# Kernel tuning notes

Hardware: AMD Instinct MI355X
Metric: run time of the kernel (lower is better)

## Reference

```python
import jax, jax.numpy as jnp
import numpy as np

B, T, IN, H, OUT = 128, 512, 64, 1024, 1


def _glorot(key, shape, fan_in):
    # mimic nn.Linear default init scale (uniform +-1/sqrt(fan_in))
    bound = 1.0 / np.sqrt(fan_in)
    return jax.random.uniform(key, shape, jnp.float32, -bound, bound)


def setup_inputs() -> dict:
    key = jax.random.key(0)
    ks = jax.random.split(key, 20)
    inp = {
        "x": jax.random.normal(ks[0], (B, T, IN), jnp.float32),
        "boundary": jax.random.normal(ks[1], (B, 2), jnp.float32),
        # layer 0: stacked gate weights, order [i, f, o, g]
        "Wx0": _glorot(ks[2], (4 * H, IN), IN),
        "bx0": _glorot(ks[3], (4 * H,), IN),
        "Uh0": _glorot(ks[4], (4 * H, H), H),
        "bh0": _glorot(ks[5], (4 * H,), H),
        "Wb0": _glorot(ks[6], (H, 2), 2),
        "bb0": _glorot(ks[7], (H,), 2),
        # layer 1
        "Wx1": _glorot(ks[8], (4 * H, H), H),
        "bx1": _glorot(ks[9], (4 * H,), H),
        "Uh1": _glorot(ks[10], (4 * H, H), H),
        "bh1": _glorot(ks[11], (4 * H,), H),
        "Wb1": _glorot(ks[12], (H, 2), 2),
        "bb1": _glorot(ks[13], (H, 2)[:1], 2),
        # output head
        "fcW": _glorot(ks[14], (OUT, H), H),
        "fcb": _glorot(ks[15], (OUT,), H),
    }
    return inp


def _cell(gates, f_extra, c_prev):
    # gates: [B, 4H] pre-activations in order i,f,o,g
    i, f, o, g = jnp.split(gates, 4, axis=-1)
    i = jax.nn.sigmoid(i)
    f = jax.nn.sigmoid(f + f_extra)
    o = jax.nn.sigmoid(o)
    g = jnp.tanh(g)
    c = f * c_prev + i * g
    h = o * jnp.tanh(c)
    return h, c


def reference(x, boundary, Wx0, bx0, Uh0, bh0, Wb0, bb0,
              Wx1, bx1, Uh1, bh1, Wb1, bb1, fcW, fcb):
    batch = x.shape[0]
    Hdim = fcW.shape[1]
    # precompute input projections for layer 0 over all timesteps: [T,B,4H]
    xp0 = jnp.einsum('bti,gi->tbg', x, Wx0) + bx0
    # boundary influence on forget gate, constant over time: [B,H]
    bi0 = boundary @ Wb0.T + bb0
    bi1 = boundary @ Wb1.T + bb1

    zeros = jnp.zeros((batch, Hdim), x.dtype)
    carry0 = (zeros, zeros, zeros, zeros)  # h0, c0, h1, c1

    def step(carry, xp_t):
        h0, c0, h1, c1 = carry
        g0 = xp_t + h0 @ Uh0.T + bh0
        h0n, c0n = _cell(g0, bi0, c0)
        g1 = h0n @ Wx1.T + bx1 + h1 @ Uh1.T + bh1
        h1n, c1n = _cell(g1, bi1, c1)
        return (h0n, c0n, h1n, c1n), None

    (h0, c0, h1, c1), _ = jax.lax.scan(step, carry0, xp0)
    # fc applied to last timestep's top-layer hidden state
    return h1 @ fcW.T + fcb
```

## Files before the change

### kernel.cpp

```cpp
#include <hip/hip_runtime.h>
#include <math.h>


#define Hd 1024
#define Bd 128
#define Td 512
#define INd 64
#define NWG 256
#define NTHR 512

typedef _Float16 f16;
typedef _Float16 half8 __attribute__((ext_vector_type(8)));
typedef float f32x4 __attribute__((ext_vector_type(4)));


__global__ __launch_bounds__(512) void init_state(
    const float* __restrict__ bnd, const float* __restrict__ Wb0,
    const float* __restrict__ bb0, const float* __restrict__ Wb1,
    const float* __restrict__ bb1,
    float* __restrict__ bi0, float* __restrict__ bi1,
    f16* __restrict__ h0buf, f16* __restrict__ h1buf,
    unsigned int* __restrict__ sync)
{
    int idx = blockIdx.x * 512 + threadIdx.x;
    int b = idx >> 10;
    int h = idx & 1023;
    float b0v = bnd[b * 2 + 0], b1v = bnd[b * 2 + 1];
    bi0[idx] = b0v * Wb0[h * 2 + 0] + b1v * Wb0[h * 2 + 1] + bb0[h];
    bi1[idx] = b0v * Wb1[h * 2 + 0] + b1v * Wb1[h * 2 + 1] + bb1[h];
    h0buf[idx] = (f16)0.f;  h0buf[idx + Bd * Hd] = (f16)0.f;
    h1buf[idx] = (f16)0.f;  h1buf[idx + Bd * Hd] = (f16)0.f;
    if (idx < 640) sync[idx] = 0u;
}

__global__ __launch_bounds__(512) void xpose(
    const float* __restrict__ x, f16* __restrict__ xT)
{
    int idx = blockIdx.x * 512 + threadIdx.x;
    int b = idx >> 15;
    int t = (idx >> 6) & 511;
    int i = idx & 63;
    xT[((size_t)t * Bd + b) * INd + i] = (f16)x[idx];
}

__global__ __launch_bounds__(NTHR, 2) void lstm_persist(
    const f16* __restrict__ xT,
    f16* __restrict__ h0buf, f16* __restrict__ h1buf,
    const float* __restrict__ bi0, const float* __restrict__ bi1,
    const float* __restrict__ Wx0, const float* __restrict__ bx0,
    const float* __restrict__ Uh0, const float* __restrict__ bh0,
    const float* __restrict__ Wx1, const float* __restrict__ bx1,
    const float* __restrict__ Uh1, const float* __restrict__ bh1,
    const float* __restrict__ fcW, const float* __restrict__ fcb,
    float* __restrict__ out, unsigned int* __restrict__ sync)
{
    const int tid  = threadIdx.x;
    const int w    = tid >> 6;
    const int lane = tid & 63;
    const int n    = lane & 15;
    const int q    = lane >> 4;
    const int wg   = blockIdx.x;
    const int c0wg = wg * 4;
    const int hcol = c0wg + (n & 3);
    const int gid  = n >> 2;
    const bool lowhalf = (w < 4);
    const int p    = lowhalf ? w : (w - 4);
    const int mt   = lowhalf ? 2 * p : 2 * p + 1;
    const size_t S = (size_t)Bd * Hd;

    __shared__ f16 B0[16 * 1096];
    __shared__ float xchg[3072];

    const bool glead = ((wg & 31) == 0);
    unsigned int* garr = sync + 32 + 32 * (wg >> 5);
    int  xcd  = 0;
    bool lead = false;
    unsigned int* relp = nullptr;
    if (tid == 0) {
        asm volatile("s_getreg_b32 %0, hwreg(HW_REG_XCC_ID)" : "=s"(xcd));
        xcd &= 7;
        unsigned r = __hip_atomic_fetch_add(&sync[608 + xcd], 1u,
                         __ATOMIC_RELAXED, __HIP_MEMORY_SCOPE_AGENT);
        lead = (r == 0u);
        relp = sync + 288 + 32 * xcd;
    }

    {
        int nr = tid >> 5;
        int gr = (nr >> 2) * Hd + c0wg + (nr & 3);
        for (int k = tid & 31; k < 1088; k += 32) {
            float v = (k < Hd) ? Uh0[(size_t)gr * Hd + k]
                               : Wx0[(size_t)gr * INd + (k - Hd)];
            B0[nr * 1096 + k] = (f16)v;
        }
    }

    half8 b1f[32];
    {
        const float* Wsrc = lowhalf ? Wx1 : Uh1;
        int gr = gid * Hd + c0wg + (n & 3);
        const float* rp = Wsrc + (size_t)gr * Hd + q * 8;
        #pragma unroll
        for (int kk = 0; kk < 32; ++kk) {
            half8 hv;
            #pragma unroll
            for (int j = 0; j < 8; ++j) hv[j] = (f16)rp[kk * 32 + j];
            b1f[kk] = hv;
        }
    }

    float gb0[4], gb1[4], bia0[4], bia1[4];
    #pragma unroll
    for (int g = 0; g < 4; ++g) {
        gb0[g] = bx0[g * Hd + hcol] + bh0[g * Hd + hcol];
        gb1[g] = bx1[g * Hd + hcol] + bh1[g * Hd + hcol];
    }
    #pragma unroll
    for (int r = 0; r < 4; ++r) {
        int row = mt * 16 + q * 4 + r;
        bia0[r] = bi0[row * Hd + hcol];
        bia1[r] = bi1[row * Hd + hcol];
    }
    f32x4 c0v = {0.f, 0.f, 0.f, 0.f};
    f32x4 c1v = {0.f, 0.f, 0.f, 0.f};

    __syncthreads();

    unsigned epoch = 0;

    for (int s = -1; s <= 511; ++s) {
        const bool do_l0 = (s < 511);
        const bool do_l1 = (s >= 0);
        const int pr = s & 1;
        const f16* h0r = h0buf + (size_t)pr * S;
        f16*       h0w = h0buf + (size_t)(1 - pr) * S;
        const f16* h1r = h1buf + (size_t)(1 - pr) * S;
        f16*       h1w = h1buf + (size_t)pr * S;

        f32x4 a0a = {0.f,0.f,0.f,0.f}, a0b = {0.f,0.f,0.f,0.f};
        f32x4 a1a = {0.f,0.f,0.f,0.f}, a1b = {0.f,0.f,0.f,0.f};

        if (lowhalf) {
            const half8* pA0 = (const half8*)(h0r + (size_t)(2*p*16 + n) * Hd + q*8);
            const half8* pA1 = (const half8*)(h0r + (size_t)((2*p+1)*16 + n) * Hd + q*8);
            const half8* pB  = (const half8*)(&B0[n * 1096 + q * 8]);
            if (do_l0 && do_l1) {
                #pragma unroll
                for (int kk = 0; kk < 32; ++kk) {
                    half8 A0 = pA0[kk*4], A1 = pA1[kk*4], Bl = pB[kk*4];
                    a0a = __builtin_amdgcn_mfma_f32_16x16x32_f16(A0, Bl, a0a, 0,0,0);
                    a0b = __builtin_amdgcn_mfma_f32_16x16x32_f16(A1, Bl, a0b, 0,0,0);
                    a1a = __builtin_amdgcn_mfma_f32_16x16x32_f16(A0, b1f[kk], a1a, 0,0,0);
                    a1b = __builtin_amdgcn_mfma_f32_16x16x32_f16(A1, b1f[kk], a1b, 0,0,0);
                }
            } else if (do_l0) {
                #pragma unroll
                for (int kk = 0; kk < 32; ++kk) {
                    half8 A0 = pA0[kk*4], A1 = pA1[kk*4], Bl = pB[kk*4];
                    a0a = __builtin_amdgcn_mfma_f32_16x16x32_f16(A0, Bl, a0a, 0,0,0);
                    a0b = __builtin_amdgcn_mfma_f32_16x16x32_f16(A1, Bl, a0b, 0,0,0);
                }
            } else {
                #pragma unroll
                for (int kk = 0; kk < 32; ++kk) {
                    half8 A0 = pA0[kk*4], A1 = pA1[kk*4];
                    a1a = __builtin_amdgcn_mfma_f32_16x16x32_f16(A0, b1f[kk], a1a, 0,0,0);
                    a1b = __builtin_amdgcn_mfma_f32_16x16x32_f16(A1, b1f[kk], a1b, 0,0,0);
                }
            }
            if (do_l0) {
                const f16* xt = xT + (size_t)(s + 1) * Bd * INd;
                const half8* pX0 = (const half8*)(xt + (size_t)(2*p*16 + n) * INd + q*8);
                const half8* pX1 = (const half8*)(xt + (size_t)((2*p+1)*16 + n) * INd + q*8);
                #pragma unroll
                for (int kk = 0; kk < 2; ++kk) {
                    half8 Bl = pB[(32 + kk) * 4];
                    a0a = __builtin_amdgcn_mfma_f32_16x16x32_f16(pX0[kk*4], Bl, a0a, 0,0,0);
                    a0b = __builtin_amdgcn_mfma_f32_16x16x32_f16(pX1[kk*4], Bl, a0b, 0,0,0);
                }
            }
        } else if (do_l1) {
            const half8* pH1a = (const half8*)(h1r + (size_t)(2*p*16 + n) * Hd + q*8);
            const half8* pH1b = (const half8*)(h1r + (size_t)((2*p+1)*16 + n) * Hd + q*8);
            #pragma unroll
            for (int kk = 0; kk < 32; ++kk) {
                half8 A0 = pH1a[kk*4], A1 = pH1b[kk*4];
                a1a = __builtin_amdgcn_mfma_f32_16x16x32_f16(A0, b1f[kk], a1a, 0,0,0);
                a1b = __builtin_amdgcn_mfma_f32_16x16x32_f16(A1, b1f[kk], a1b, 0,0,0);
            }
        }

        float* slotA = xchg;
        float* slotB = xchg + 1024;
        float* slotC = xchg + 2048;
        if (lowhalf) {
            if (do_l0) *(f32x4*)&slotA[p * 256 + lane * 4] = a0b;
            if (do_l1) *(f32x4*)&slotB[p * 256 + lane * 4] = a1b;
        } else {
            if (do_l1) *(f32x4*)&slotC[p * 256 + lane * 4] = a1a;
        }
        __syncthreads();

        f32x4 g0acc, g1acc;
        if (lowhalf) {
            g0acc = a0a;
            if (do_l1) g1acc = a1a + *(const f32x4*)&slotC[p * 256 + lane * 4];
        } else {
            if (do_l0) g0acc = *(const f32x4*)&slotA[p * 256 + lane * 4];
            if (do_l1) g1acc = a1b + *(const f32x4*)&slotB[p * 256 + lane * 4];
        }

        auto cell = [&](f32x4 acc, const float* gb, const float* bia,
                        f32x4& cst, f16* hw) {
            #pragma unroll
            for (int r = 0; r < 4; ++r) {
                float own = acc[r];
                float v4  = __shfl_xor(own, 4);
                float v8  = __shfl_xor(own, 8);
                float v12 = __shfl_xor(own, 12);
                float ip = gid==0?own: gid==1?v4 : gid==2?v8 : v12;
                float fp = gid==0?v4 : gid==1?own: gid==2?v12: v8;
                float op = gid==0?v8 : gid==1?v12: gid==2?own: v4;
                float gp = gid==0?v12: gid==1?v8 : gid==2?v4 : own;
                float I = 1.f / (1.f + expf(-(ip + gb[0])));
                float F = 1.f / (1.f + expf(-(fp + gb[1] + bia[r])));
                float O = 1.f / (1.f + expf(-(op + gb[2])));
                float G = tanhf(gp + gb[3]);
                float c = F * cst[r] + I * G;
                cst[r] = c;
                float h = O * tanhf(c);
                if (n < 4) {
                    union { f16 hf; unsigned short us; } cv; cv.hf = (f16)h;
                    __hip_atomic_store(
                        (unsigned short*)&hw[(size_t)(mt * 16 + q * 4 + r) * Hd + c0wg + n],
                        cv.us, __ATOMIC_RELAXED, __HIP_MEMORY_SCOPE_AGENT);
                }
            }
        };
        if (do_l0) cell(g0acc, gb0, bia0, c0v, h0w);
        if (do_l1) cell(g1acc, gb1, bia1, c1v, h1w);

        __syncthreads();
        if (tid == 0) {
            const unsigned tgt = epoch + 1u;
            __hip_atomic_fetch_add(garr, 1u, __ATOMIC_RELAXED,
                                   __HIP_MEMORY_SCOPE_AGENT);
            if (glead) {
                while (__hip_atomic_load(garr, __ATOMIC_RELAXED,
                                         __HIP_MEMORY_SCOPE_AGENT) < 32u * tgt)
                    __builtin_amdgcn_s_sleep(1);
                __hip_atomic_fetch_add(sync, 32u, __ATOMIC_RELAXED,
                                       __HIP_MEMORY_SCOPE_AGENT);
            }
            if (lead) {
                while (__hip_atomic_load(sync, __ATOMIC_RELAXED,
                                         __HIP_MEMORY_SCOPE_AGENT) < NWG * tgt)
                    __builtin_amdgcn_s_sleep(1);
                asm volatile("buffer_inv sc1\n\ts_waitcnt vmcnt(0)" ::: "memory");
                __hip_atomic_store(relp, tgt, __ATOMIC_RELAXED,
                                   __HIP_MEMORY_SCOPE_AGENT);
            } else {
                while (__hip_atomic_load(relp, __ATOMIC_RELAXED,
                                         __HIP_MEMORY_SCOPE_AGENT) < tgt)
                    __builtin_amdgcn_s_sleep(1);
                asm volatile("buffer_inv\n\ts_waitcnt vmcnt(0)" ::: "memory");
            }
        }
        epoch++;
        __syncthreads();
    }

    if (blockIdx.x < Bd) {
        int b = blockIdx.x;
        const f16* hf = h1buf + S + (size_t)b * Hd;
        int k = tid * 2;
        float sum = (float)hf[k] * fcW[k] + (float)hf[k + 1] * fcW[k + 1];
        #pragma unroll
        for (int off = 32; off > 0; off >>= 1) sum += __shfl_down(sum, off);
        float* red = xchg;
        if (lane == 0) red[w] = sum;
        __syncthreads();
        if (tid == 0) {
            float t = 0.f;
            #pragma unroll
            for (int i = 0; i < 8; ++i) t += red[i];
            out[b] = t + fcb[0];
        }
    }
}

extern "C" void kernel_launch(void* const* d_in, const int* in_sizes, int n_in,
                              void* d_out, int out_size, void* d_ws, size_t ws_size,
                              hipStream_t stream) {
    const float* x        = (const float*)d_in[0];
    const float* boundary = (const float*)d_in[1];
    const float* Wx0      = (const float*)d_in[2];
    const float* bx0      = (const float*)d_in[3];
    const float* Uh0      = (const float*)d_in[4];
    const float* bh0      = (const float*)d_in[5];
    const float* Wb0      = (const float*)d_in[6];
    const float* bb0      = (const float*)d_in[7];
    const float* Wx1      = (const float*)d_in[8];
    const float* bx1      = (const float*)d_in[9];
    const float* Uh1      = (const float*)d_in[10];
    const float* bh1      = (const float*)d_in[11];
    const float* Wb1      = (const float*)d_in[12];
    const float* bb1      = (const float*)d_in[13];
    const float* fcW      = (const float*)d_in[14];
    const float* fcb      = (const float*)d_in[15];
    float* out = (float*)d_out;

    char* ws = (char*)d_ws;
    f16*   xT    = (f16*)(ws);
    f16*   h0buf = (f16*)(ws + 8388608);
    f16*   h1buf = (f16*)(ws + 8912896);
    float* bi0   = (float*)(ws + 9437184);
    float* bi1   = (float*)(ws + 9961472);
    unsigned int* sync = (unsigned int*)(ws + 10485760);

    init_state<<<256, 512, 0, stream>>>(boundary, Wb0, bb0, Wb1, bb1,
                                        bi0, bi1, h0buf, h1buf, sync);
    xpose<<<8192, 512, 0, stream>>>(x, xT);

    void* args[] = {
        (void*)&xT, (void*)&h0buf, (void*)&h1buf, (void*)&bi0, (void*)&bi1,
        (void*)&Wx0, (void*)&bx0, (void*)&Uh0, (void*)&bh0,
        (void*)&Wx1, (void*)&bx1, (void*)&Uh1, (void*)&bh1,
        (void*)&fcW, (void*)&fcb, (void*)&out, (void*)&sync
    };
    hipLaunchCooperativeKernel((void*)lstm_persist, dim3(NWG), dim3(NTHR),
                               args, 0, stream);
}
```

Baseline: 11.62 ms.

## Store hidden state in k-blocked layout and use fast sigmoid/tanh intrinsics

Changes the global h0/h1 exchange buffers from row-major [B][H] to a blocked [H/4][B][4] layout. Each workgroup's 4-column output slice now lands in one contiguous region, and the MFMA A-operand is built from two half4 loads. The gate nonlinearities switch from expf/tanhf to __expf/__fdividef approximations, which shortens the serial per-step cell math at some accuracy cost. The final FC readout is updated to index the new layout.

```diff
diff --git a/kernel.cpp b/kernel.cpp
--- a/kernel.cpp
+++ b/kernel.cpp
@@ -11,8 +11,16 @@
 
 typedef _Float16 f16;
 typedef _Float16 half8 __attribute__((ext_vector_type(8)));
+typedef _Float16 half4 __attribute__((ext_vector_type(4)));
 typedef float f32x4 __attribute__((ext_vector_type(4)));
 
+
+__device__ __forceinline__ float fsigm(float x) {
+    return __fdividef(1.f, 1.f + __expf(-x));
+}
+__device__ __forceinline__ float ftanh_(float x) {
+    return 1.f - __fdividef(2.f, 1.f + __expf(2.f * x));
+}
 
 __global__ __launch_bounds__(512) void init_state(
     const float* __restrict__ bnd, const float* __restrict__ Wb0,
@@ -128,6 +136,9 @@
 
     unsigned epoch = 0;
 
+    const int ra = 2 * p * 16 + n;
+    const int rb = (2 * p + 1) * 16 + n;
+
     for (int s = -1; s <= 511; ++s) {
         const bool do_l0 = (s < 511);
         const bool do_l1 = (s >= 0);
@@ -141,13 +152,19 @@
         f32x4 a1a = {0.f,0.f,0.f,0.f}, a1b = {0.f,0.f,0.f,0.f};
 
         if (lowhalf) {
-            const half8* pA0 = (const half8*)(h0r + (size_t)(2*p*16 + n) * Hd + q*8);
-            const half8* pA1 = (const half8*)(h0r + (size_t)((2*p+1)*16 + n) * Hd + q*8);
+            const half4* hb = (const half4*)h0r;
             const half8* pB  = (const half8*)(&B0[n * 1096 + q * 8]);
             if (do_l0 && do_l1) {
                 #pragma unroll
                 for (int kk = 0; kk < 32; ++kk) {
-                    half8 A0 = pA0[kk*4], A1 = pA1[kk*4], Bl = pB[kk*4];
+                    int kb = q * 2 + kk * 8;
+                    half4 a0lo = hb[(kb    ) * 128 + ra];
+                    half4 a0hi = hb[(kb + 1) * 128 + ra];
+                    half4 a1lo = hb[(kb    ) * 128 + rb];
+                    half4 a1hi = hb[(kb + 1) * 128 + rb];
+                    half8 A0 = __builtin_shufflevector(a0lo, a0hi, 0,1,2,3,4,5,6,7);
+                    half8 A1 = __builtin_shufflevector(a1lo, a1hi, 0,1,2,3,4,5,6,7);
+                    half8 Bl = pB[kk*4];
                     a0a = __builtin_amdgcn_mfma_f32_16x16x32_f16(A0, Bl, a0a, 0,0,0);
                     a0b = __builtin_amdgcn_mfma_f32_16x16x32_f16(A1, Bl, a0b, 0,0,0);
                     a1a = __builtin_amdgcn_mfma_f32_16x16x32_f16(A0, b1f[kk], a1a, 0,0,0);
@@ -156,14 +173,27 @@
             } else if (do_l0) {
                 #pragma unroll
                 for (int kk = 0; kk < 32; ++kk) {
-                    half8 A0 = pA0[kk*4], A1 = pA1[kk*4], Bl = pB[kk*4];
+                    int kb = q * 2 + kk * 8;
+                    half4 a0lo = hb[(kb    ) * 128 + ra];
+                    half4 a0hi = hb[(kb + 1) * 128 + ra];
+                    half4 a1lo = hb[(kb    ) * 128 + rb];
+                    half4 a1hi = hb[(kb + 1) * 128 + rb];
+                    half8 A0 = __builtin_shufflevector(a0lo, a0hi, 0,1,2,3,4,5,6,7);
+                    half8 A1 = __builtin_shufflevector(a1lo, a1hi, 0,1,2,3,4,5,6,7);
+                    half8 Bl = pB[kk*4];
                     a0a = __builtin_amdgcn_mfma_f32_16x16x32_f16(A0, Bl, a0a, 0,0,0);
                     a0b = __builtin_amdgcn_mfma_f32_16x16x32_f16(A1, Bl, a0b, 0,0,0);
                 }
             } else {
                 #pragma unroll
                 for (int kk = 0; kk < 32; ++kk) {
-                    half8 A0 = pA0[kk*4], A1 = pA1[kk*4];
+                    int kb = q * 2 + kk * 8;
+                    half4 a0lo = hb[(kb    ) * 128 + ra];
+                    half4 a0hi = hb[(kb + 1) * 128 + ra];
+                    half4 a1lo = hb[(kb    ) * 128 + rb];
+                    half4 a1hi = hb[(kb + 1) * 128 + rb];
+                    half8 A0 = __builtin_shufflevector(a0lo, a0hi, 0,1,2,3,4,5,6,7);
+                    half8 A1 = __builtin_shufflevector(a1lo, a1hi, 0,1,2,3,4,5,6,7);
                     a1a = __builtin_amdgcn_mfma_f32_16x16x32_f16(A0, b1f[kk], a1a, 0,0,0);
                     a1b = __builtin_amdgcn_mfma_f32_16x16x32_f16(A1, b1f[kk], a1b, 0,0,0);
                 }
@@ -180,11 +210,16 @@
                 }
             }
         } else if (do_l1) {
-            const half8* pH1a = (const half8*)(h1r + (size_t)(2*p*16 + n) * Hd + q*8);
-            const half8* pH1b = (const half8*)(h1r + (size_t)((2*p+1)*16 + n) * Hd + q*8);
+            const half4* hb = (const half4*)h1r;
             #pragma unroll
             for (int kk = 0; kk < 32; ++kk) {
-                half8 A0 = pH1a[kk*4], A1 = pH1b[kk*4];
+                int kb = q * 2 + kk * 8;
+                half4 a0lo = hb[(kb    ) * 128 + ra];
+                half4 a0hi = hb[(kb + 1) * 128 + ra];
+                half4 a1lo = hb[(kb    ) * 128 + rb];
+                half4 a1hi = hb[(kb + 1) * 128 + rb];
+                half8 A0 = __builtin_shufflevector(a0lo, a0hi, 0,1,2,3,4,5,6,7);
+                half8 A1 = __builtin_shufflevector(a1lo, a1hi, 0,1,2,3,4,5,6,7);
                 a1a = __builtin_amdgcn_mfma_f32_16x16x32_f16(A0, b1f[kk], a1a, 0,0,0);
                 a1b = __builtin_amdgcn_mfma_f32_16x16x32_f16(A1, b1f[kk], a1b, 0,0,0);
             }
@@ -222,17 +257,17 @@
                 float fp = gid==0?v4 : gid==1?own: gid==2?v12: v8;
                 float op = gid==0?v8 : gid==1?v12: gid==2?own: v4;
                 float gp = gid==0?v12: gid==1?v8 : gid==2?v4 : own;
-                float I = 1.f / (1.f + expf(-(ip + gb[0])));
-                float F = 1.f / (1.f + expf(-(fp + gb[1] + bia[r])));
-                float O = 1.f / (1.f + expf(-(op + gb[2])));
-                float G = tanhf(gp + gb[3]);
+                float I = fsigm(ip + gb[0]);
+                float F = fsigm(fp + gb[1] + bia[r]);
+                float O = fsigm(op + gb[2]);
+                float G = ftanh_(gp + gb[3]);
                 float c = F * cst[r] + I * G;
                 cst[r] = c;
-                float h = O * tanhf(c);
+                float h = O * ftanh_(c);
                 if (n < 4) {
                     union { f16 hf; unsigned short us; } cv; cv.hf = (f16)h;
                     __hip_atomic_store(
-                        (unsigned short*)&hw[(size_t)(mt * 16 + q * 4 + r) * Hd + c0wg + n],
+                        (unsigned short*)&hw[(size_t)(wg * 128 + mt * 16 + q * 4 + r) * 4 + n],
                         cv.us, __ATOMIC_RELAXED, __HIP_MEMORY_SCOPE_AGENT);
                 }
             }
@@ -272,9 +307,10 @@
 
     if (blockIdx.x < Bd) {
         int b = blockIdx.x;
-        const f16* hf = h1buf + S + (size_t)b * Hd;
+        const f16* hf = h1buf + S;
         int k = tid * 2;
-        float sum = (float)hf[k] * fcW[k] + (float)hf[k + 1] * fcW[k + 1];
+        int idx = (((k >> 2) * 128 + b) << 2) + (k & 3);
+        float sum = (float)hf[idx] * fcW[k] + (float)hf[idx + 1] * fcW[k + 1];
         #pragma unroll
         for (int off = 32; off > 0; off >>= 1) sum += __shfl_down(sum, off);
         float* red = xchg;
```

Result: slower. 20.17 ms (+73.7%).
